# Performance work log

Hardware: AMD Instinct MI355X
Metric: run time of the kernel (lower is better)

## Reference

```python
import jax, jax.numpy as jnp
import numpy as np

EPS = 1e-10

def norm_t(x, axis):
    # zero-mean + L2 normalize along `axis` (standard NCC normalization)
    xc = x - jnp.mean(x, axis=axis, keepdims=True)
    return xc / (jnp.linalg.norm(xc, axis=axis, keepdims=True) + EPS)

def setup_inputs() -> dict:
    key = jax.random.key(0)
    k1, k2 = jax.random.split(key)
    input_compressed = jax.random.normal(k1, (1, 16, 131072), dtype=jnp.float32)  # [B, K, N]
    cmat = jax.random.normal(k2, (16, 1024), dtype=jnp.float32)                   # [K, D]
    return {"input_compressed": input_compressed, "cmat": cmat}

def reference(input_compressed, cmat):
    a = norm_t(input_compressed, axis=-2)          # [B, K, N], normalized over K
    b = norm_t(cmat, axis=0)                       # [K, D],    normalized over K
    ncc = jnp.einsum('bkn,kd->bnd', a, b)          # [B, N, D] correlation volume
    # torch: argmax(transpose(ncc,-2,-1), dim=-2) -> argmax over D -> [B, N]
    pred_depths = jnp.argmax(ncc, axis=-1)         # [B, N] int depth-bin indices
    return pred_depths
```

## Files before the change

### kernel.cpp

```cpp
#include <hip/hip_runtime.h>
#include <hip/hip_bf16.h>
#include <math.h>

#define N_PTS  131072
#define K_DIM  16
#define D_BINS 1024
#define MARGIN_P 6e-4f

typedef short bf16x8 __attribute__((ext_vector_type(8)));
typedef float f32x4  __attribute__((ext_vector_type(4)));

#define WS_OFF_BN  64
#define WS_OFF_B   65600
#define WS_OFF_WL  131136
#define WS_NEED    655424

__device__ __forceinline__ void norm_np(const float* __restrict__ p,
                                        int stride, int n, float* __restrict__ a) {
#pragma clang fp contract(off)
    float v[K_DIM];
#pragma unroll
    for (int k = 0; k < K_DIM; ++k) v[k] = p[(size_t)k * stride + n];
    float s = v[0];
#pragma unroll
    for (int k = 1; k < K_DIM; ++k) s = s + v[k];
    const float mean = s / 16.0f;
    float sq[K_DIM];
#pragma unroll
    for (int k = 0; k < K_DIM; ++k) { a[k] = v[k] - mean; sq[k] = a[k] * a[k]; }
    float ss = sq[0];
#pragma unroll
    for (int k = 1; k < K_DIM; ++k) ss = ss + sq[k];
    const float denom = sqrtf(ss) + 1e-10f;
#pragma unroll
    for (int k = 0; k < K_DIM; ++k) a[k] = a[k] / denom;
}

__device__ __forceinline__ unsigned short bf16_bits(float f) {
    __hip_bfloat16 h = __float2bfloat16(f);
    unsigned short u;
    __builtin_memcpy(&u, &h, 2);
    return u;
}
__device__ __forceinline__ float bf16_val(float f) {
    return __bfloat162float(__float2bfloat16(f));
}

__global__ __launch_bounds__(256) void prep_b(
    const float* __restrict__ cmat, float* __restrict__ bnT,
    unsigned short* __restrict__ B1, int* __restrict__ wl_count) {
#pragma clang fp contract(off)
    if (blockIdx.x == 0 && threadIdx.x == 0) *wl_count = 0;
    const int d = blockIdx.x * 256 + threadIdx.x;
    if (d >= D_BINS) return;

    float t[K_DIM];
    norm_np(cmat, D_BINS, d, t);

    unsigned short* B2 = B1 + 16384;
    const int tile = d >> 4, n = d & 15;
#pragma unroll
    for (int k = 0; k < K_DIM; ++k) {
        bnT[d * K_DIM + k] = t[k];
        const float hi_f = bf16_val(t[k]);
        const int idx = tile * 256 + ((k >> 3) * 16 + n) * 8 + (k & 7);
        B1[idx] = bf16_bits(t[k]);
        B2[idx] = bf16_bits(t[k] - hi_f);
    }
}

__global__ __launch_bounds__(512) void mfma_screen(
    const float* __restrict__ x, const unsigned short* __restrict__ Bpack,
    int* __restrict__ out, int* __restrict__ wl, int* __restrict__ wl_count) {
#pragma clang fp contract(off)
    __shared__ float4 ldsB[4097];

    {
        const float4* src = (const float4*)Bpack;
#pragma unroll
        for (int j = 0; j < 8; ++j)
            ldsB[threadIdx.x + j * 512] = src[threadIdx.x + j * 512];
        if (threadIdx.x == 0) ldsB[4096] = (float4){0.f, 0.f, 0.f, 0.f};
    }

    const int lane = threadIdx.x & 63;
    const int wv   = threadIdx.x >> 6;
    const int W    = blockIdx.x * 8 + wv;
    const int P    = W * 32;
    const int m    = lane & 15;
    const int q    = lane >> 4;

    bf16x8 A[2];
#pragma unroll
    for (int t = 0; t < 2; ++t) {
        float a[K_DIM];
        norm_np(x, N_PTS, P + t * 16 + m, a);
        unsigned short els[8];
#pragma unroll
        for (int j = 0; j < 8; ++j) {
            const int k = (q & 1) * 8 + j;
            if (q < 2) els[j] = bf16_bits(a[k]);
            else       els[j] = bf16_bits(a[k] - bf16_val(a[k]));
        }
        __builtin_memcpy(&A[t], els, 16);
    }

    __syncthreads();

    const char* lb = (const char*)ldsB;
    const char* b1p = lb + (size_t)(lane & 31) * 16;
    const char* b2p = (lane < 32) ? (lb + 32768 + (size_t)lane * 16) : (lb + 65536);
    const int   b2s = (lane < 32) ? 512 : 0;

    unsigned ub1[2][4], ub2[2][4];
#pragma unroll
    for (int t = 0; t < 2; ++t)
#pragma unroll
        for (int r = 0; r < 4; ++r) { ub1[t][r] = 0u; ub2[t][r] = 0u; }

    const unsigned mask = 0xFFFFF800u;

    for (int i = 0; i < 64; ++i) {
        bf16x8 bf1, bf2;
        __builtin_memcpy(&bf1, b1p + (size_t)i * 512, 16);
        __builtin_memcpy(&bf2, b2p + (size_t)i * b2s, 16);

        f32x4 acc[2];
#pragma unroll
        for (int t = 0; t < 2; ++t)
            acc[t] = __builtin_amdgcn_mfma_f32_16x16x32_bf16(
                A[t], bf1, (f32x4){2.f, 2.f, 2.f, 2.f}, 0, 0, 0);
#pragma unroll
        for (int t = 0; t < 2; ++t)
            acc[t] = __builtin_amdgcn_mfma_f32_16x16x32_bf16(
                A[t], bf2, acc[t], 0, 0, 0);

        const unsigned dcomp = 2047u - (unsigned)(i * 16 + m);
#pragma unroll
        for (int t = 0; t < 2; ++t)
#pragma unroll
            for (int r = 0; r < 4; ++r) {
                const unsigned u = (__float_as_uint(acc[t][r]) & mask) | dcomp;
                const unsigned nx = max(ub1[t][r], u);
                ub2[t][r] = max(ub2[t][r], min(ub1[t][r], u));
                ub1[t][r] = nx;
            }
    }

#pragma unroll
    for (int t = 0; t < 2; ++t)
#pragma unroll
        for (int r = 0; r < 4; ++r) {
            unsigned u1 = ub1[t][r], u2 = ub2[t][r];
#pragma unroll
            for (int s = 1; s <= 8; s <<= 1) {
                const unsigned o1 = (unsigned)__shfl_xor((int)u1, s, 16);
                const unsigned o2 = (unsigned)__shfl_xor((int)u2, s, 16);
                const unsigned n1 = max(u1, o1);
                u2 = max(min(u1, o1), max(u2, o2));
                u1 = n1;
            }
            if (m == 0) {
                const int p  = P + t * 16 + q * 4 + r;
                const float s1 = __uint_as_float(u1 & mask);
                const float s2 = __uint_as_float(u2 & mask);
                if (s1 - s2 > MARGIN_P) {
                    out[p] = 2047 - (int)(u1 & 2047u);
                } else {
                    const int pos = atomicAdd(wl_count, 1);
                    wl[pos] = p;
                }
            }
        }
}

__global__ __launch_bounds__(256) void ncc_exact_refine(
    const float* __restrict__ x, const float* __restrict__ bnT,
    int* __restrict__ out, const int* __restrict__ wl,
    const int* __restrict__ wl_count) {
#pragma clang fp contract(off)
    const int count  = *wl_count;
    const int lane   = threadIdx.x & 63;
    const int wave   = (blockIdx.x * 256 + threadIdx.x) >> 6;
    const int nwaves = (gridDim.x * 256) >> 6;

    for (int i = wave; i < count; i += nwaves) {
        const int n = wl[i];
        float a[K_DIM];
        norm_np(x, N_PTS, n, a);

        float best = -3.402823466e38f;
        int   idx  = 0x7fffffff;
        const float4* b4 = (const float4*)bnT;
        for (int t = 0; t < 16; ++t) {
            const int d = t * 64 + lane;
            const float4 q0 = b4[d * 4 + 0];
            const float4 q1 = b4[d * 4 + 1];
            const float4 q2 = b4[d * 4 + 2];
            const float4 q3 = b4[d * 4 + 3];
            float sc;
            sc = a[0] * q0.x;
            sc = sc + a[1]  * q0.y; sc = sc + a[2]  * q0.z; sc = sc + a[3]  * q0.w;
            sc = sc + a[4]  * q1.x; sc = sc + a[5]  * q1.y; sc = sc + a[6]  * q1.z;
            sc = sc + a[7]  * q1.w; sc = sc + a[8]  * q2.x; sc = sc + a[9]  * q2.y;
            sc = sc + a[10] * q2.z; sc = sc + a[11] * q2.w; sc = sc + a[12] * q3.x;
            sc = sc + a[13] * q3.y; sc = sc + a[14] * q3.z; sc = sc + a[15] * q3.w;
            if (sc > best) { best = sc; idx = d; }
        }
#pragma unroll
        for (int mk = 1; mk <= 32; mk <<= 1) {
            const float ob = __shfl_xor(best, mk);
            const int   oi = __shfl_xor(idx,  mk);
            if (ob > best || (ob == best && oi < idx)) { best = ob; idx = oi; }
        }
        if (lane == 0) out[n] = idx;
    }
}

__global__ __launch_bounds__(256) void ncc_argmax_np32(
    const float* __restrict__ x, const float* __restrict__ bnT,
    int* __restrict__ out) {
#pragma clang fp contract(off)
    const int n = blockIdx.x * 256 + threadIdx.x;
    float a[K_DIM];
    norm_np(x, N_PTS, n, a);

    float best = -3.402823466e38f;
    int   idx  = 0;
    const float4* b4 = (const float4*)bnT;
#pragma unroll 2
    for (int d = 0; d < D_BINS; ++d) {
        const float4 q0 = b4[d * 4 + 0];
        const float4 q1 = b4[d * 4 + 1];
        const float4 q2 = b4[d * 4 + 2];
        const float4 q3 = b4[d * 4 + 3];
        float sc;
        sc = a[0] * q0.x;
        sc = sc + a[1]  * q0.y; sc = sc + a[2]  * q0.z; sc = sc + a[3]  * q0.w;
        sc = sc + a[4]  * q1.x; sc = sc + a[5]  * q1.y; sc = sc + a[6]  * q1.z;
        sc = sc + a[7]  * q1.w; sc = sc + a[8]  * q2.x; sc = sc + a[9]  * q2.y;
        sc = sc + a[10] * q2.z; sc = sc + a[11] * q2.w; sc = sc + a[12] * q3.x;
        sc = sc + a[13] * q3.y; sc = sc + a[14] * q3.z; sc = sc + a[15] * q3.w;
        if (sc > best) { best = sc; idx = d; }
    }
    out[n] = idx;
}

__global__ __launch_bounds__(256) void normalize_rows_only(
    const float* __restrict__ cmat, float* __restrict__ bnT) {
#pragma clang fp contract(off)
    const int d = blockIdx.x * 256 + threadIdx.x;
    if (d >= D_BINS) return;
    float t[K_DIM];
    norm_np(cmat, D_BINS, d, t);
#pragma unroll
    for (int k = 0; k < K_DIM; ++k) bnT[d * K_DIM + k] = t[k];
}

extern "C" void kernel_launch(void* const* d_in, const int* in_sizes, int n_in,
                              void* d_out, int out_size, void* d_ws, size_t ws_size,
                              hipStream_t stream) {
    const float* x    = (const float*)d_in[0];
    const float* cmat = (const float*)d_in[1];
    int* out = (int*)d_out;
    char* ws = (char*)d_ws;

    if (ws_size >= (size_t)WS_NEED) {
        int*            wl_count = (int*)ws;
        float*          bnT      = (float*)(ws + WS_OFF_BN);
        unsigned short* Bpack    = (unsigned short*)(ws + WS_OFF_B);
        int*            wl       = (int*)(ws + WS_OFF_WL);

        prep_b<<<4, 256, 0, stream>>>(cmat, bnT, Bpack, wl_count);
        mfma_screen<<<512, 512, 0, stream>>>(x, Bpack, out, wl, wl_count);
        ncc_exact_refine<<<512, 256, 0, stream>>>(x, bnT, out, wl, wl_count);
    } else {
        float* bnT = (float*)(ws + WS_OFF_BN);
        normalize_rows_only<<<4, 256, 0, stream>>>(cmat, bnT);
        ncc_argmax_np32<<<512, 256, 0, stream>>>(x, bnT, out);
    }
}
```

Measured before the change: 108.8 us.

## Halve points per wave, stage only hi B tile in LDS, read lo from global

The screening kernel now handles 16 points per wave instead of 32 and launches twice as many blocks. Only the high bf16 part of the normalized cmat is staged in shared memory (32KB instead of 64KB), while the low-part correction is read straight from global memory or a small zero block. The aim is higher occupancy from less LDS and fewer registers per wave, plus a launch-bounds hint for 8 waves. The cost is that each block reloads B1, and the lo fragments now come through the cache hierarchy instead of LDS, with half the MFMA reuse per B load.

Result: no change. 108.9 us (+0.2%).

```diff
diff --git a/kernel.cpp b/kernel.cpp
--- a/kernel.cpp
+++ b/kernel.cpp
@@ -11,9 +11,11 @@
 typedef float f32x4  __attribute__((ext_vector_type(4)));
 
 #define WS_OFF_BN  64
-#define WS_OFF_B   65600
-#define WS_OFF_WL  131136
-#define WS_NEED    655424
+#define WS_OFF_B1  65600
+#define WS_OFF_B2  98368
+#define WS_OFF_Z   131136
+#define WS_OFF_WL  131152
+#define WS_NEED    655440
 
 __device__ __forceinline__ void norm_np(const float* __restrict__ p,
                                         int stride, int n, float* __restrict__ a) {
@@ -48,16 +50,19 @@
 
 __global__ __launch_bounds__(256) void prep_b(
     const float* __restrict__ cmat, float* __restrict__ bnT,
-    unsigned short* __restrict__ B1, int* __restrict__ wl_count) {
-#pragma clang fp contract(off)
-    if (blockIdx.x == 0 && threadIdx.x == 0) *wl_count = 0;
+    unsigned short* __restrict__ B1, unsigned short* __restrict__ B2,
+    unsigned short* __restrict__ zblk, int* __restrict__ wl_count) {
+#pragma clang fp contract(off)
+    if (blockIdx.x == 0) {
+        if (threadIdx.x == 0) *wl_count = 0;
+        if (threadIdx.x < 8) zblk[threadIdx.x] = 0;
+    }
     const int d = blockIdx.x * 256 + threadIdx.x;
     if (d >= D_BINS) return;
 
     float t[K_DIM];
     norm_np(cmat, D_BINS, d, t);
 
-    unsigned short* B2 = B1 + 16384;
     const int tile = d >> 4, n = d & 15;
 #pragma unroll
     for (int k = 0; k < K_DIM; ++k) {
@@ -69,32 +74,31 @@
     }
 }
 
-__global__ __launch_bounds__(512) void mfma_screen(
-    const float* __restrict__ x, const unsigned short* __restrict__ Bpack,
+__global__ __launch_bounds__(512, 8) void mfma_screen(
+    const float* __restrict__ x, const unsigned short* __restrict__ B1,
+    const unsigned short* __restrict__ B2, const unsigned short* __restrict__ zblk,
     int* __restrict__ out, int* __restrict__ wl, int* __restrict__ wl_count) {
 #pragma clang fp contract(off)
-    __shared__ float4 ldsB[4097];
+    __shared__ float4 ldsB[2048];
 
     {
-        const float4* src = (const float4*)Bpack;
-#pragma unroll
-        for (int j = 0; j < 8; ++j)
+        const float4* src = (const float4*)B1;
+#pragma unroll
+        for (int j = 0; j < 4; ++j)
             ldsB[threadIdx.x + j * 512] = src[threadIdx.x + j * 512];
-        if (threadIdx.x == 0) ldsB[4096] = (float4){0.f, 0.f, 0.f, 0.f};
     }
 
     const int lane = threadIdx.x & 63;
     const int wv   = threadIdx.x >> 6;
     const int W    = blockIdx.x * 8 + wv;
-    const int P    = W * 32;
+    const int P    = W * 16;
     const int m    = lane & 15;
     const int q    = lane >> 4;
 
-    bf16x8 A[2];
-#pragma unroll
-    for (int t = 0; t < 2; ++t) {
+    bf16x8 A;
+    {
         float a[K_DIM];
-        norm_np(x, N_PTS, P + t * 16 + m, a);
+        norm_np(x, N_PTS, P + m, a);
         unsigned short els[8];
 #pragma unroll
         for (int j = 0; j < 8; ++j) {
@@ -102,21 +106,19 @@
             if (q < 2) els[j] = bf16_bits(a[k]);
             else       els[j] = bf16_bits(a[k] - bf16_val(a[k]));
         }
-        __builtin_memcpy(&A[t], els, 16);
+        __builtin_memcpy(&A, els, 16);
     }
 
     __syncthreads();
 
-    const char* lb = (const char*)ldsB;
-    const char* b1p = lb + (size_t)(lane & 31) * 16;
-    const char* b2p = (lane < 32) ? (lb + 32768 + (size_t)lane * 16) : (lb + 65536);
+    const char* b1p = (const char*)ldsB + (size_t)(lane & 31) * 16;
+    const char* b2p = (lane < 32) ? ((const char*)B2 + (size_t)lane * 16)
+                                  : (const char*)zblk;
     const int   b2s = (lane < 32) ? 512 : 0;
 
-    unsigned ub1[2][4], ub2[2][4];
-#pragma unroll
-    for (int t = 0; t < 2; ++t)
-#pragma unroll
-        for (int r = 0; r < 4; ++r) { ub1[t][r] = 0u; ub2[t][r] = 0u; }
+    unsigned ub1[4], ub2[4];
+#pragma unroll
+    for (int r = 0; r < 4; ++r) { ub1[r] = 0u; ub2[r] = 0u; }
 
     const unsigned mask = 0xFFFFF800u;
 
@@ -125,53 +127,43 @@
         __builtin_memcpy(&bf1, b1p + (size_t)i * 512, 16);
         __builtin_memcpy(&bf2, b2p + (size_t)i * b2s, 16);
 
-        f32x4 acc[2];
-#pragma unroll
-        for (int t = 0; t < 2; ++t)
-            acc[t] = __builtin_amdgcn_mfma_f32_16x16x32_bf16(
-                A[t], bf1, (f32x4){2.f, 2.f, 2.f, 2.f}, 0, 0, 0);
-#pragma unroll
-        for (int t = 0; t < 2; ++t)
-            acc[t] = __builtin_amdgcn_mfma_f32_16x16x32_bf16(
-                A[t], bf2, acc[t], 0, 0, 0);
+        f32x4 acc = __builtin_amdgcn_mfma_f32_16x16x32_bf16(
+            A, bf1, (f32x4){2.f, 2.f, 2.f, 2.f}, 0, 0, 0);
+        acc = __builtin_amdgcn_mfma_f32_16x16x32_bf16(A, bf2, acc, 0, 0, 0);
 
         const unsigned dcomp = 2047u - (unsigned)(i * 16 + m);
 #pragma unroll
-        for (int t = 0; t < 2; ++t)
-#pragma unroll
-            for (int r = 0; r < 4; ++r) {
-                const unsigned u = (__float_as_uint(acc[t][r]) & mask) | dcomp;
-                const unsigned nx = max(ub1[t][r], u);
-                ub2[t][r] = max(ub2[t][r], min(ub1[t][r], u));
-                ub1[t][r] = nx;
+        for (int r = 0; r < 4; ++r) {
+            const unsigned u = (__float_as_uint(acc[r]) & mask) | dcomp;
+            const unsigned nx = max(ub1[r], u);
+            ub2[r] = max(ub2[r], min(ub1[r], u));
+            ub1[r] = nx;
+        }
+    }
+
+#pragma unroll
+    for (int r = 0; r < 4; ++r) {
+        unsigned u1 = ub1[r], u2 = ub2[r];
+#pragma unroll
+        for (int s = 1; s <= 8; s <<= 1) {
+            const unsigned o1 = (unsigned)__shfl_xor((int)u1, s, 16);
+            const unsigned o2 = (unsigned)__shfl_xor((int)u2, s, 16);
+            const unsigned n1 = max(u1, o1);
+            u2 = max(min(u1, o1), max(u2, o2));
+            u1 = n1;
+        }
+        if (m == 0) {
+            const int p  = P + q * 4 + r;
+            const float s1 = __uint_as_float(u1 & mask);
+            const float s2 = __uint_as_float(u2 & mask);
+            if (s1 - s2 > MARGIN_P) {
+                out[p] = 2047 - (int)(u1 & 2047u);
+            } else {
+                const int pos = atomicAdd(wl_count, 1);
+                wl[pos] = p;
             }
-    }
-
-#pragma unroll
-    for (int t = 0; t < 2; ++t)
-#pragma unroll
-        for (int r = 0; r < 4; ++r) {
-            unsigned u1 = ub1[t][r], u2 = ub2[t][r];
-#pragma unroll
-            for (int s = 1; s <= 8; s <<= 1) {
-                const unsigned o1 = (unsigned)__shfl_xor((int)u1, s, 16);
-                const unsigned o2 = (unsigned)__shfl_xor((int)u2, s, 16);
-                const unsigned n1 = max(u1, o1);
-                u2 = max(min(u1, o1), max(u2, o2));
-                u1 = n1;
-            }
-            if (m == 0) {
-                const int p  = P + t * 16 + q * 4 + r;
-                const float s1 = __uint_as_float(u1 & mask);
-                const float s2 = __uint_as_float(u2 & mask);
-                if (s1 - s2 > MARGIN_P) {
-                    out[p] = 2047 - (int)(u1 & 2047u);
-                } else {
-                    const int pos = atomicAdd(wl_count, 1);
-                    wl[pos] = p;
-                }
-            }
-        }
+        }
+    }
 }
 
 __global__ __launch_bounds__(256) void ncc_exact_refine(
@@ -268,11 +260,13 @@
     if (ws_size >= (size_t)WS_NEED) {
         int*            wl_count = (int*)ws;
         float*          bnT      = (float*)(ws + WS_OFF_BN);
-        unsigned short* Bpack    = (unsigned short*)(ws + WS_OFF_B);
+        unsigned short* B1       = (unsigned short*)(ws + WS_OFF_B1);
+        unsigned short* B2       = (unsigned short*)(ws + WS_OFF_B2);
+        unsigned short* zblk     = (unsigned short*)(ws + WS_OFF_Z);
         int*            wl       = (int*)(ws + WS_OFF_WL);
 
-        prep_b<<<4, 256, 0, stream>>>(cmat, bnT, Bpack, wl_count);
-        mfma_screen<<<512, 512, 0, stream>>>(x, Bpack, out, wl, wl_count);
+        prep_b<<<4, 256, 0, stream>>>(cmat, bnT, B1, B2, zblk, wl_count);
+        mfma_screen<<<1024, 512, 0, stream>>>(x, B1, B2, zblk, out, wl, wl_count);
         ncc_exact_refine<<<512, 256, 0, stream>>>(x, bnT, out, wl, wl_count);
     } else {
         float* bnT = (float*)(ws + WS_OFF_BN);
```

## Fuse exact refinement into MFMA screen with single-bf16 B and per-block worklist

Applied to the files above, without the earlier changes.

Drops the bf16 lo-part of the depth matrix so each iteration runs two MFMAs instead of four, and widens the acceptance margin to make up for the coarser screen. Ambiguous points now go into a per-block shared-memory list and are refined exactly inside the same kernel. This removes the global atomic worklist and the separate refine launch. In exchange, more points may need refinement, and a block that overflows its 128-entry list falls back to refining all 256 of its points serially, which can leave blocks unevenly loaded.

New measurement: 141.3 us. 1.3x slower.

```diff
diff --git a/kernel.cpp b/kernel.cpp
--- a/kernel.cpp
+++ b/kernel.cpp
@@ -5,15 +5,14 @@
 #define N_PTS  131072
 #define K_DIM  16
 #define D_BINS 1024
-#define MARGIN_P 6e-4f
+#define MARGIN_P 5e-3f
 
 typedef short bf16x8 __attribute__((ext_vector_type(8)));
 typedef float f32x4  __attribute__((ext_vector_type(4)));
 
-#define WS_OFF_BN  64
-#define WS_OFF_B   65600
-#define WS_OFF_WL  131136
-#define WS_NEED    655424
+#define WS_OFF_BN  0
+#define WS_OFF_BH  65536
+#define WS_NEED    98304
 
 __device__ __forceinline__ void norm_np(const float* __restrict__ p,
                                         int stride, int n, float* __restrict__ a) {
@@ -46,51 +45,81 @@
     return __bfloat162float(__float2bfloat16(f));
 }
 
+__device__ __forceinline__ void refine_point(
+    const float* __restrict__ x, const float* __restrict__ bnT,
+    int* __restrict__ out, int n, int lane) {
+#pragma clang fp contract(off)
+    float a[K_DIM];
+    norm_np(x, N_PTS, n, a);
+
+    float best = -3.402823466e38f;
+    int   idx  = 0x7fffffff;
+    const float4* b4 = (const float4*)bnT;
+    for (int t = 0; t < 16; ++t) {
+        const int d = t * 64 + lane;
+        const float4 q0 = b4[d * 4 + 0];
+        const float4 q1 = b4[d * 4 + 1];
+        const float4 q2 = b4[d * 4 + 2];
+        const float4 q3 = b4[d * 4 + 3];
+        float sc;
+        sc = a[0] * q0.x;
+        sc = sc + a[1]  * q0.y; sc = sc + a[2]  * q0.z; sc = sc + a[3]  * q0.w;
+        sc = sc + a[4]  * q1.x; sc = sc + a[5]  * q1.y; sc = sc + a[6]  * q1.z;
+        sc = sc + a[7]  * q1.w; sc = sc + a[8]  * q2.x; sc = sc + a[9]  * q2.y;
+        sc = sc + a[10] * q2.z; sc = sc + a[11] * q2.w; sc = sc + a[12] * q3.x;
+        sc = sc + a[13] * q3.y; sc = sc + a[14] * q3.z; sc = sc + a[15] * q3.w;
+        if (sc > best) { best = sc; idx = d; }
+    }
+#pragma unroll
+    for (int mk = 1; mk <= 32; mk <<= 1) {
+        const float ob = __shfl_xor(best, mk);
+        const int   oi = __shfl_xor(idx,  mk);
+        if (ob > best || (ob == best && oi < idx)) { best = ob; idx = oi; }
+    }
+    if (lane == 0) out[n] = idx;
+}
+
 __global__ __launch_bounds__(256) void prep_b(
     const float* __restrict__ cmat, float* __restrict__ bnT,
-    unsigned short* __restrict__ B1, int* __restrict__ wl_count) {
-#pragma clang fp contract(off)
-    if (blockIdx.x == 0 && threadIdx.x == 0) *wl_count = 0;
+    unsigned short* __restrict__ Bh) {
+#pragma clang fp contract(off)
     const int d = blockIdx.x * 256 + threadIdx.x;
     if (d >= D_BINS) return;
 
     float t[K_DIM];
     norm_np(cmat, D_BINS, d, t);
 
-    unsigned short* B2 = B1 + 16384;
     const int tile = d >> 4, n = d & 15;
 #pragma unroll
     for (int k = 0; k < K_DIM; ++k) {
         bnT[d * K_DIM + k] = t[k];
-        const float hi_f = bf16_val(t[k]);
         const int idx = tile * 256 + ((k >> 3) * 16 + n) * 8 + (k & 7);
-        B1[idx] = bf16_bits(t[k]);
-        B2[idx] = bf16_bits(t[k] - hi_f);
-    }
-}
-
-__global__ __launch_bounds__(512) void mfma_screen(
-    const float* __restrict__ x, const unsigned short* __restrict__ Bpack,
-    int* __restrict__ out, int* __restrict__ wl, int* __restrict__ wl_count) {
-#pragma clang fp contract(off)
-    __shared__ float4 ldsB[4097];
-
+        Bh[idx] = bf16_bits(t[k]);
+    }
+}
+
+__global__ __launch_bounds__(512, 4) void mfma_screen(
+    const float* __restrict__ x, const uint4* __restrict__ Bh,
+    const float* __restrict__ bnT, int* __restrict__ out) {
+#pragma clang fp contract(off)
+    __shared__ uint4 ldsB[2048];
+    __shared__ int s_cnt;
+    __shared__ int s_list[128];
+
+    if (threadIdx.x == 0) s_cnt = 0;
     {
-        const float4* src = (const float4*)Bpack;
-#pragma unroll
-        for (int j = 0; j < 8; ++j)
-            ldsB[threadIdx.x + j * 512] = src[threadIdx.x + j * 512];
-        if (threadIdx.x == 0) ldsB[4096] = (float4){0.f, 0.f, 0.f, 0.f};
+#pragma unroll
+        for (int j = 0; j < 4; ++j)
+            ldsB[threadIdx.x + j * 512] = Bh[threadIdx.x + j * 512];
     }
 
     const int lane = threadIdx.x & 63;
     const int wv   = threadIdx.x >> 6;
-    const int W    = blockIdx.x * 8 + wv;
-    const int P    = W * 32;
+    const int P    = (blockIdx.x * 8 + wv) * 32;
     const int m    = lane & 15;
     const int q    = lane >> 4;
 
-    bf16x8 A[2];
+    bf16x8 A0, A1;
 #pragma unroll
     for (int t = 0; t < 2; ++t) {
         float a[K_DIM];
@@ -102,15 +131,13 @@
             if (q < 2) els[j] = bf16_bits(a[k]);
             else       els[j] = bf16_bits(a[k] - bf16_val(a[k]));
         }
-        __builtin_memcpy(&A[t], els, 16);
+        if (t == 0) __builtin_memcpy(&A0, els, 16);
+        else        __builtin_memcpy(&A1, els, 16);
     }
 
     __syncthreads();
 
-    const char* lb = (const char*)ldsB;
-    const char* b1p = lb + (size_t)(lane & 31) * 16;
-    const char* b2p = (lane < 32) ? (lb + 32768 + (size_t)lane * 16) : (lb + 65536);
-    const int   b2s = (lane < 32) ? 512 : 0;
+    const uint4* bp = ldsB + (lane & 31);
 
     unsigned ub1[2][4], ub2[2][4];
 #pragma unroll
@@ -118,24 +145,20 @@
 #pragma unroll
         for (int r = 0; r < 4; ++r) { ub1[t][r] = 0u; ub2[t][r] = 0u; }
 
-    const unsigned mask = 0xFFFFF800u;
-
+    const unsigned mask  = 0xFFFFF800u;
+    const unsigned dbase = 2047u - (unsigned)m;
+
+#pragma unroll 4
     for (int i = 0; i < 64; ++i) {
-        bf16x8 bf1, bf2;
-        __builtin_memcpy(&bf1, b1p + (size_t)i * 512, 16);
-        __builtin_memcpy(&bf2, b2p + (size_t)i * b2s, 16);
+        const bf16x8 bf = __builtin_bit_cast(bf16x8, bp[i * 32]);
 
         f32x4 acc[2];
-#pragma unroll
-        for (int t = 0; t < 2; ++t)
-            acc[t] = __builtin_amdgcn_mfma_f32_16x16x32_bf16(
-                A[t], bf1, (f32x4){2.f, 2.f, 2.f, 2.f}, 0, 0, 0);
-#pragma unroll
-        for (int t = 0; t < 2; ++t)
-            acc[t] = __builtin_amdgcn_mfma_f32_16x16x32_bf16(
-                A[t], bf2, acc[t], 0, 0, 0);
-
-        const unsigned dcomp = 2047u - (unsigned)(i * 16 + m);
+        acc[0] = __builtin_amdgcn_mfma_f32_16x16x32_bf16(
+            A0, bf, (f32x4){2.f, 2.f, 2.f, 2.f}, 0, 0, 0);
+        acc[1] = __builtin_amdgcn_mfma_f32_16x16x32_bf16(
+            A1, bf, (f32x4){2.f, 2.f, 2.f, 2.f}, 0, 0, 0);
+
+        const unsigned dcomp = dbase - (unsigned)(i * 16);
 #pragma unroll
         for (int t = 0; t < 2; ++t)
 #pragma unroll
@@ -167,53 +190,20 @@
                 if (s1 - s2 > MARGIN_P) {
                     out[p] = 2047 - (int)(u1 & 2047u);
                 } else {
-                    const int pos = atomicAdd(wl_count, 1);
-                    wl[pos] = p;
+                    const int pos = atomicAdd(&s_cnt, 1);
+                    if (pos < 128) s_list[pos] = p;
                 }
             }
         }
-}
-
-__global__ __launch_bounds__(256) void ncc_exact_refine(
-    const float* __restrict__ x, const float* __restrict__ bnT,
-    int* __restrict__ out, const int* __restrict__ wl,
-    const int* __restrict__ wl_count) {
-#pragma clang fp contract(off)
-    const int count  = *wl_count;
-    const int lane   = threadIdx.x & 63;
-    const int wave   = (blockIdx.x * 256 + threadIdx.x) >> 6;
-    const int nwaves = (gridDim.x * 256) >> 6;
-
-    for (int i = wave; i < count; i += nwaves) {
-        const int n = wl[i];
-        float a[K_DIM];
-        norm_np(x, N_PTS, n, a);
-
-        float best = -3.402823466e38f;
-        int   idx  = 0x7fffffff;
-        const float4* b4 = (const float4*)bnT;
-        for (int t = 0; t < 16; ++t) {
-            const int d = t * 64 + lane;
-            const float4 q0 = b4[d * 4 + 0];
-            const float4 q1 = b4[d * 4 + 1];
-            const float4 q2 = b4[d * 4 + 2];
-            const float4 q3 = b4[d * 4 + 3];
-            float sc;
-            sc = a[0] * q0.x;
-            sc = sc + a[1]  * q0.y; sc = sc + a[2]  * q0.z; sc = sc + a[3]  * q0.w;
-            sc = sc + a[4]  * q1.x; sc = sc + a[5]  * q1.y; sc = sc + a[6]  * q1.z;
-            sc = sc + a[7]  * q1.w; sc = sc + a[8]  * q2.x; sc = sc + a[9]  * q2.y;
-            sc = sc + a[10] * q2.z; sc = sc + a[11] * q2.w; sc = sc + a[12] * q3.x;
-            sc = sc + a[13] * q3.y; sc = sc + a[14] * q3.z; sc = sc + a[15] * q3.w;
-            if (sc > best) { best = sc; idx = d; }
-        }
-#pragma unroll
-        for (int mk = 1; mk <= 32; mk <<= 1) {
-            const float ob = __shfl_xor(best, mk);
-            const int   oi = __shfl_xor(idx,  mk);
-            if (ob > best || (ob == best && oi < idx)) { best = ob; idx = oi; }
-        }
-        if (lane == 0) out[n] = idx;
+
+    __syncthreads();
+    const int c = s_cnt;
+    if (c <= 128) {
+        for (int i = wv; i < c; i += 8)
+            refine_point(x, bnT, out, s_list[i], lane);
+    } else {
+        for (int i = wv; i < 256; i += 8)
+            refine_point(x, bnT, out, blockIdx.x * 256 + i, lane);
     }
 }
 
@@ -265,17 +255,14 @@
     int* out = (int*)d_out;
     char* ws = (char*)d_ws;
 
+    float*          bnT = (float*)(ws + WS_OFF_BN);
+    unsigned short* Bh  = (unsigned short*)(ws + WS_OFF_BH);
+
     if (ws_size >= (size_t)WS_NEED) {
-        int*            wl_count = (int*)ws;
-        float*          bnT      = (float*)(ws + WS_OFF_BN);
-        unsigned short* Bpack    = (unsigned short*)(ws + WS_OFF_B);
-        int*            wl       = (int*)(ws + WS_OFF_WL);
-
-        prep_b<<<4, 256, 0, stream>>>(cmat, bnT, Bpack, wl_count);
-        mfma_screen<<<512, 512, 0, stream>>>(x, Bpack, out, wl, wl_count);
-        ncc_exact_refine<<<512, 256, 0, stream>>>(x, bnT, out, wl, wl_count);
+        prep_b<<<4, 256, 0, stream>>>(cmat, bnT, Bh);
+        mfma_screen<<<512, 512, 0, stream>>>(
+            x, (const uint4*)(ws + WS_OFF_BH), bnT, out);
     } else {
-        float* bnT = (float*)(ws + WS_OFF_BN);
         normalize_rows_only<<<4, 256, 0, stream>>>(cmat, bnT);
         ncc_argmax_np32<<<512, 256, 0, stream>>>(x, bnT, out);
     }
```
